# Kernel tuning notes

Hardware: AMD Instinct MI355X
Metric: run time of the kernel (lower is better)

Reference implementation:

```python
import jax, jax.numpy as jnp
import numpy as np

L = 5          # num_layer
D = 256        # emb_dim
N = 50000      # nodes
E = 800000     # edges
NUM_ATOM_FEATS, ATOM_VOCAB = 9, 120
NUM_BOND_FEATS, BOND_VOCAB = 3, 6
BN_EPS = 1e-5


def setup_inputs() -> dict:
    key = jax.random.key(0)
    ks = jax.random.split(key, 16)
    s = 0.02
    inp = {
        "x": jax.random.randint(ks[0], (N, NUM_ATOM_FEATS), 0, ATOM_VOCAB),
        "edge_index": jax.random.randint(ks[1], (2, E), 0, N),
        "edge_attr": jax.random.randint(ks[2], (E, NUM_BOND_FEATS), 0, BOND_VOCAB),
        "atom_emb": jax.random.normal(ks[3], (NUM_ATOM_FEATS, ATOM_VOCAB, D), jnp.float32) * s,
        "bond_emb": jax.random.normal(ks[4], (L, NUM_BOND_FEATS, BOND_VOCAB, D), jnp.float32) * s,
        "eps": jnp.zeros((L,), jnp.float32),
        "W1": jax.random.normal(ks[5], (L, D, 2 * D), jnp.float32) * s,
        "b1": jnp.zeros((L, 2 * D), jnp.float32),
        "g1": jnp.ones((L, 2 * D), jnp.float32),
        "be1": jnp.zeros((L, 2 * D), jnp.float32),
        "W2": jax.random.normal(ks[6], (L, 2 * D, D), jnp.float32) * s,
        "b2": jnp.zeros((L, D), jnp.float32),
        "g2": jnp.ones((L, D), jnp.float32),
        "be2": jnp.zeros((L, D), jnp.float32),
    }
    return inp


def _batchnorm(h, g, b):
    # training-mode BatchNorm1d over the node dimension
    m = jnp.mean(h, axis=0)
    v = jnp.mean(jnp.square(h - m), axis=0)
    return (h - m) * jax.lax.rsqrt(v + BN_EPS) * g + b


def reference(x, edge_index, edge_attr, atom_emb, bond_emb, eps,
              W1, b1, g1, be1, W2, b2, g2, be2):
    # AtomEncoder: sum of per-feature embedding lookups -> [N, D]
    h = jnp.sum(
        jnp.stack([atom_emb[f][x[:, f]] for f in range(NUM_ATOM_FEATS)], 0), 0)
    src, dst = edge_index[0], edge_index[1]
    for l in range(L):
        # BondEncoder for this layer -> [E, D]
        e = jnp.sum(jnp.stack(
            [bond_emb[l, f][edge_attr[:, f]] for f in range(NUM_BOND_FEATS)], 0), 0)
        msg = jax.nn.relu(h[src] + e)                          # gather + transform
        agg = jax.ops.segment_sum(msg, dst, num_segments=N)   # scatter-add
        z = (1.0 + eps[l]) * h + agg
        z = _batchnorm(z @ W1[l] + b1[l], g1[l], be1[l])       # MLP hidden + BN
        z = jax.nn.relu(z) @ W2[l] + b2[l]
        z = _batchnorm(z, g2[l], be2[l])                       # outer BN
        if l < L - 1:
            z = jax.nn.relu(z)
        h = z
    return h  # JK='last', drop_ratio=0
```

## Files before the change

### kernel.cpp

```cpp
#include <hip/hip_runtime.h>
#include <stdint.h>

#define NODES 50000
#define EDGES 800000
#define EMB   256
#define MPAD  50048
#define BNEPS 1e-5f
#define SCANB 196

typedef unsigned short u16;
typedef unsigned int   u32;
typedef _Float16 f16;
typedef __attribute__((ext_vector_type(4))) _Float16 f16x4;
typedef __attribute__((ext_vector_type(8))) _Float16 f16x8;
typedef __attribute__((ext_vector_type(4))) float f32x4;


__global__ void k_w1t(const float* __restrict__ W1, f16* __restrict__ Wt){
  int i = blockIdx.x * 256 + threadIdx.x;
  if (i >= 5*512*256) return;
  int k = i & 255, n = (i >> 8) & 511, l = i >> 17;
  Wt[i] = (f16)W1[((size_t)l << 17) + ((size_t)k << 9) + n];
}
__global__ void k_w2t(const float* __restrict__ W2, f16* __restrict__ Wt){
  int i = blockIdx.x * 256 + threadIdx.x;
  if (i >= 5*256*512) return;
  int k = i & 511, n = (i >> 9) & 255, l = i >> 17;
  Wt[i] = (f16)W2[((size_t)l << 17) + ((size_t)k << 8) + n];
}

__global__ void k_ebond(const float* __restrict__ bemb, f16* __restrict__ eb){
  int l = blockIdx.x / 216, p = blockIdx.x % 216;
  int a0 = p % 6, a1 = (p / 6) % 6, a2 = p / 36;
  int d0 = threadIdx.x * 4;
  const float* b = bemb + (size_t)l * 3 * 6 * 256;
  float4 v0 = *(const float4*)(b + (0*6 + a0)*256 + d0);
  float4 v1 = *(const float4*)(b + (1*6 + a1)*256 + d0);
  float4 v2 = *(const float4*)(b + (2*6 + a2)*256 + d0);
  f16x4 o = {(f16)(v0.x+v1.x+v2.x), (f16)(v0.y+v1.y+v2.y),
             (f16)(v0.z+v1.z+v2.z), (f16)(v0.w+v1.w+v2.w)};
  *(f16x4*)(eb + (((size_t)l*216 + p) << 8) + d0) = o;
}

__global__ void k_atom(const int* __restrict__ x, const float* __restrict__ aemb,
                       f16* __restrict__ h){
  int n = blockIdx.x * 4 + (threadIdx.x >> 6);
  int lane = threadIdx.x & 63;
  if (n >= NODES) return;
  int d0 = lane * 4;
  float a0=0.f, a1=0.f, a2=0.f, a3=0.f;
#pragma unroll
  for (int f = 0; f < 9; ++f){
    int v = x[n*9 + f];
    float4 e = *(const float4*)(aemb + (((size_t)f*120 + v) << 8) + d0);
    a0 += e.x; a1 += e.y; a2 += e.z; a3 += e.w;
  }
  f16x4 o = {(f16)a0, (f16)a1, (f16)a2, (f16)a3};
  *(f16x4*)(h + (size_t)n*EMB + d0) = o;
}


__global__ void k_hist(const int* __restrict__ dst, int* __restrict__ counts){
  int e = blockIdx.x * 256 + threadIdx.x;
  if (e < EDGES) atomicAdd(&counts[dst[e]], 1);
}

__global__ void k_bsum(const int* __restrict__ counts, int* __restrict__ bsums){
  __shared__ int red[256];
  int t = threadIdx.x;
  int i = blockIdx.x * 256 + t;
  red[t] = (i < NODES) ? counts[i] : 0;
  __syncthreads();
  for (int off = 128; off > 0; off >>= 1){
    if (t < off) red[t] += red[t + off];
    __syncthreads();
  }
  if (t == 0) bsums[blockIdx.x] = red[0];
}

__global__ void k_bscan(int* __restrict__ bsums){
  __shared__ int sc[256];
  int t = threadIdx.x;
  int v = (t < SCANB) ? bsums[t] : 0;
  sc[t] = v;
  __syncthreads();
  for (int off = 1; off < 256; off <<= 1){
    int u = (t >= off) ? sc[t - off] : 0;
    __syncthreads();
    sc[t] += u;
    __syncthreads();
  }
  if (t < SCANB) bsums[t] = sc[t] - v;
}

__global__ void k_fill(const int* __restrict__ counts, const int* __restrict__ bsums,
                       int* __restrict__ rs, int* __restrict__ fill){
  __shared__ int sc[256];
  int t = threadIdx.x;
  int i = blockIdx.x * 256 + t;
  int v = (i < NODES) ? counts[i] : 0;
  sc[t] = v;
  __syncthreads();
  for (int off = 1; off < 256; off <<= 1){
    int u = (t >= off) ? sc[t - off] : 0;
    __syncthreads();
    sc[t] += u;
    __syncthreads();
  }
  if (i < NODES){
    int e = bsums[blockIdx.x] + sc[t] - v;
    rs[i] = e; fill[i] = e;
    if (i == NODES - 1) rs[NODES] = e + v;
  }
}

__global__ void k_scatter(const int* __restrict__ src, const int* __restrict__ dst,
                          const int* __restrict__ ea, int* __restrict__ fill,
                          int* __restrict__ csrc, int* __restrict__ cattr){
  int e = blockIdx.x * 256 + threadIdx.x;
  if (e >= EDGES) return;
  int d = dst[e];
  int p = atomicAdd(&fill[d], 1);
  csrc[p]  = src[e];
  cattr[p] = ea[e*3+0] + 6*ea[e*3+1] + 36*ea[e*3+2];
}


__global__ void k_gather(const f16* __restrict__ h, const f16* __restrict__ ebl,
                         const int* __restrict__ rs, const int* __restrict__ csrc,
                         const int* __restrict__ cattr, const float* __restrict__ epsv,
                         int layer, f16* __restrict__ z){
  int n = blockIdx.x * 4 + (threadIdx.x >> 6);
  int lane = threadIdx.x & 63;
  int half = lane >> 5;
  int dl = (lane & 31) * 8;
  if (n >= MPAD) return;
  if (n >= NODES){
    if (half == 0){
      f16x8 zz = {(f16)0.f,(f16)0.f,(f16)0.f,(f16)0.f,(f16)0.f,(f16)0.f,(f16)0.f,(f16)0.f};
      *(f16x8*)(z + (size_t)n*EMB + dl) = zz;
    }
    return;
  }
  float acc[8];
#pragma unroll
  for (int k = 0; k < 8; ++k) acc[k] = 0.f;
  int i1 = rs[n+1];
  int i  = rs[n] + half;
  bool v = i < i1;
  int s = 0, pa = 0;
  if (v){ s = csrc[i]; pa = cattr[i]; }
  while (v){
    f16x8 hv = *(const f16x8*)(h + (size_t)s*EMB + dl);
    f16x8 ev = *(const f16x8*)(ebl + ((size_t)pa << 8) + dl);
    int in = i + 2;
    bool vn = in < i1;
    int sn = 0, pan = 0;
    if (vn){ sn = csrc[in]; pan = cattr[in]; }
#pragma unroll
    for (int k = 0; k < 8; ++k)
      acc[k] += fmaxf((float)hv[k] + (float)ev[k], 0.f);
    i = in; s = sn; pa = pan; v = vn;
  }
#pragma unroll
  for (int k = 0; k < 8; ++k) acc[k] += __shfl_xor(acc[k], 32);
  if (half == 0){
    float ep = 1.0f + epsv[layer];
    f16x8 hv = *(const f16x8*)(h + (size_t)n*EMB + dl);
    f16x8 o;
#pragma unroll
    for (int k = 0; k < 8; ++k) o[k] = (f16)(acc[k] + ep*(float)hv[k]);
    *(f16x8*)(z + (size_t)n*EMB + dl) = o;
  }
}

template<int K, int NCOL, bool FUSEBN>
__global__ __launch_bounds__(256)
void k_gemm(const f16* __restrict__ A, const f16* __restrict__ Bt,
            const f16* __restrict__ bnsc, const f16* __restrict__ bnsh,
            f16* __restrict__ C, float* __restrict__ csum, float* __restrict__ csq){
  const int tid  = threadIdx.x;
  const int lane = tid & 63;
  const int wid  = tid >> 6;
  const int bm0 = blockIdx.x * 128;
  const int bn0 = blockIdx.y * 128;
  const int wm = (wid >> 1) * 64;
  const int wn = (wid & 1) * 64;
  const int lr = lane & 15;
  const int kc = (lane >> 4) * 8;

  const f16* Ap = A  + (size_t)(bm0 + wm + lr)*K + kc;
  const f16* Bp = Bt + (size_t)(bn0 + wn + lr)*K + kc;

  f32x4 acc[4][4];
#pragma unroll
  for (int m = 0; m < 4; ++m)
#pragma unroll
    for (int n = 0; n < 4; ++n) acc[m][n] = (f32x4){0.f,0.f,0.f,0.f};

  const f16x8 zero8 = {(f16)0.f,(f16)0.f,(f16)0.f,(f16)0.f,
                       (f16)0.f,(f16)0.f,(f16)0.f,(f16)0.f};

#pragma unroll 2
  for (int kk = 0; kk < K/32; ++kk){
    f16x8 af[4], bf[4];
#pragma unroll
    for (int m = 0; m < 4; ++m)
      af[m] = *(const f16x8*)(Ap + (size_t)m*16*K + kk*32);
#pragma unroll
    for (int n = 0; n < 4; ++n)
      bf[n] = *(const f16x8*)(Bp + (size_t)n*16*K + kk*32);
    if (FUSEBN){
      f16x8 sc = *(const f16x8*)(bnsc + kk*32 + kc);
      f16x8 sh = *(const f16x8*)(bnsh + kk*32 + kc);
#pragma unroll
      for (int m = 0; m < 4; ++m){
        f16x8 t = af[m]*sc + sh;
#pragma unroll
        for (int j = 0; j < 8; ++j) t[j] = (t[j] > (f16)0.f) ? t[j] : (f16)0.f;
        af[m] = (bm0 + wm + m*16 + lr < NODES) ? t : zero8;
      }
    }
#pragma unroll
    for (int m = 0; m < 4; ++m)
#pragma unroll
      for (int n = 0; n < 4; ++n)
        acc[m][n] = __builtin_amdgcn_mfma_f32_16x16x32_f16(af[m], bf[n], acc[m][n], 0, 0, 0);
  }

  const int r0 = (lane >> 4) * 4;
  const int cc = lane & 15;
#pragma unroll
  for (int m = 0; m < 4; ++m)
#pragma unroll
    for (int n = 0; n < 4; ++n)
#pragma unroll
      for (int j = 0; j < 4; ++j){
        int row = bm0 + wm + m*16 + r0 + j;
        int col = bn0 + wn + n*16 + cc;
        C[(size_t)row*NCOL + col] = (f16)acc[m][n][j];
      }
#pragma unroll
  for (int n = 0; n < 4; ++n){
    float s = 0.f, q = 0.f;
#pragma unroll
    for (int m = 0; m < 4; ++m)
#pragma unroll
      for (int j = 0; j < 4; ++j){ float v = acc[m][n][j]; s += v; q += v*v; }
    s += __shfl_xor(s, 16); q += __shfl_xor(q, 16);
    s += __shfl_xor(s, 32); q += __shfl_xor(q, 32);
    if (lane < 16){
      atomicAdd(csum + bn0 + wn + n*16 + cc, s);
      atomicAdd(csq  + bn0 + wn + n*16 + cc, q);
    }
  }
}

__global__ void k_finalize(const float* __restrict__ sum, const float* __restrict__ sumsq,
                           const float* __restrict__ g, const float* __restrict__ be,
                           float* __restrict__ scale, float* __restrict__ shift,
                           f16* __restrict__ scf, f16* __restrict__ shf, int nc){
  int c = blockIdx.x * 256 + threadIdx.x;
  if (c >= nc) return;
  float m = sum[c] * (1.0f / NODES);
  float v = sumsq[c] * (1.0f / NODES) - m*m;
  float sc = rsqrtf(v + BNEPS) * g[c];
  float sh = be[c] - m*sc;
  scale[c] = sc;  shift[c] = sh;
  scf[c] = (f16)sc;  shf[c] = (f16)sh;
}

__global__ void k_apply2(const f16* __restrict__ zp, const float* __restrict__ scale,
                         const float* __restrict__ shift, f16* __restrict__ hout,
                         float* __restrict__ fout, int dorelu){
  int idx = blockIdx.x * 256 + threadIdx.x;
  int row = idx >> 5;
  int c0  = (idx & 31) * 8;
  if (row >= NODES) return;
  size_t off = (size_t)row * EMB + c0;
  f16x8 v = *(const f16x8*)(zp + off);
  float4 sA = *(const float4*)(scale + c0), sB = *(const float4*)(scale + c0 + 4);
  float4 tA = *(const float4*)(shift + c0), tB = *(const float4*)(shift + c0 + 4);
  float r0 = (float)v[0]*sA.x + tA.x;
  float r1 = (float)v[1]*sA.y + tA.y;
  float r2 = (float)v[2]*sA.z + tA.z;
  float r3 = (float)v[3]*sA.w + tA.w;
  float r4 = (float)v[4]*sB.x + tB.x;
  float r5 = (float)v[5]*sB.y + tB.y;
  float r6 = (float)v[6]*sB.z + tB.z;
  float r7 = (float)v[7]*sB.w + tB.w;
  if (dorelu){
    r0=fmaxf(r0,0.f); r1=fmaxf(r1,0.f); r2=fmaxf(r2,0.f); r3=fmaxf(r3,0.f);
    r4=fmaxf(r4,0.f); r5=fmaxf(r5,0.f); r6=fmaxf(r6,0.f); r7=fmaxf(r7,0.f);
  }
  if (fout){
    float4 f0 = {r0,r1,r2,r3}, f1 = {r4,r5,r6,r7};
    float* q = fout + off;
    *(float4*)q = f0; *(float4*)(q + 4) = f1;
  } else {
    f16x8 o = {(f16)r0,(f16)r1,(f16)r2,(f16)r3,(f16)r4,(f16)r5,(f16)r6,(f16)r7};
    *(f16x8*)(hout + off) = o;
  }
}


extern "C" void kernel_launch(void* const* d_in, const int* in_sizes, int n_in,
                              void* d_out, int out_size, void* d_ws, size_t ws_size,
                              hipStream_t stream){
  const int*   x    = (const int*)  d_in[0];
  const int*   ei   = (const int*)  d_in[1];
  const int*   ea   = (const int*)  d_in[2];
  const float* aemb = (const float*)d_in[3];
  const float* bemb = (const float*)d_in[4];
  const float* epsv = (const float*)d_in[5];
  const float* W1   = (const float*)d_in[6];
  const float* g1   = (const float*)d_in[8];
  const float* be1  = (const float*)d_in[9];
  const float* W2   = (const float*)d_in[10];
  const float* g2   = (const float*)d_in[12];
  const float* be2  = (const float*)d_in[13];
  float* out = (float*)d_out;

  char* p = (char*)d_ws;
  auto take = [&](size_t bytes){ char* r = p; p += (bytes + 255) & ~(size_t)255; return r; };
  f16* h      = (f16*)take((size_t)NODES*EMB*2);
  f16* z      = (f16*)take((size_t)MPAD*EMB*2);
  f16* hidden = (f16*)take((size_t)MPAD*512*2);
  f16* W1t    = (f16*)take((size_t)5*512*256*2);
  f16* W2t    = (f16*)take((size_t)5*256*512*2);
  f16* eb     = (f16*)take((size_t)5*216*256*2);
  float* stats= (float*)take((size_t)4*512*4);
  float* csum = stats, *csq = stats + 512, *scale = stats + 1024, *shift = stats + 1536;
  f16* scf    = (f16*)take((size_t)512*2);
  f16* shf    = (f16*)take((size_t)512*2);
  int* counts = (int*)take((size_t)NODES*4);
  int* rs     = (int*)take((size_t)(NODES+1)*4);
  int* fill   = (int*)take((size_t)NODES*4);
  int* bsums  = (int*)take((size_t)SCANB*4);
  int* csrc   = (int*)take((size_t)EDGES*4);
  int* cattr  = (int*)take((size_t)EDGES*4);

  k_w1t<<<2560, 256, 0, stream>>>(W1, W1t);
  k_w2t<<<2560, 256, 0, stream>>>(W2, W2t);
  k_ebond<<<5*216, 64, 0, stream>>>(bemb, eb);
  k_atom<<<12500, 256, 0, stream>>>(x, aemb, h);
  hipMemsetAsync(counts, 0, (size_t)NODES*4, stream);
  k_hist<<<EDGES/256, 256, 0, stream>>>(ei + EDGES, counts);
  k_bsum<<<SCANB, 256, 0, stream>>>(counts, bsums);
  k_bscan<<<1, 256, 0, stream>>>(bsums);
  k_fill<<<SCANB, 256, 0, stream>>>(counts, bsums, rs, fill);
  k_scatter<<<EDGES/256, 256, 0, stream>>>(ei, ei + EDGES, ea, fill, csrc, cattr);

  for (int l = 0; l < 5; ++l){
    k_gather<<<MPAD/4, 256, 0, stream>>>(h, eb + (size_t)l*216*256, rs, csrc, cattr, epsv, l, z);
    hipMemsetAsync(stats, 0, 2*512*4, stream);
    k_gemm<256,512,false><<<dim3(MPAD/128, 4), 256, 0, stream>>>(
        z, W1t + (size_t)l*512*256, nullptr, nullptr, hidden, csum, csq);
    k_finalize<<<2, 256, 0, stream>>>(csum, csq, g1 + l*512, be1 + l*512,
                                      scale, shift, scf, shf, 512);
    hipMemsetAsync(stats, 0, 2*512*4, stream);
    k_gemm<512,256,true><<<dim3(MPAD/128, 2), 256, 0, stream>>>(
        hidden, W2t + (size_t)l*256*512, scf, shf, z, csum, csq);
    k_finalize<<<1, 256, 0, stream>>>(csum, csq, g2 + l*256, be2 + l*256,
                                      scale, shift, scf, shf, 256);
    if (l < 4)
      k_apply2<<<NODES*32/256, 256, 0, stream>>>(z, scale, shift, h, nullptr, 1);
    else
      k_apply2<<<NODES*32/256, 256, 0, stream>>>(z, scale, shift, nullptr, out, 0);
  }
}
```

Baseline: 1.424 ms.

## Stage GEMM tiles in LDS via direct global-to-LDS loads with XOR swizzle

The GEMM kernel used to load its A and B fragments straight from global memory into registers for each wave, so waves sharing a tile fetched the same rows more than once. It now loads 128x64 tiles of A and B into shared memory with global_load_lds, using an XOR swizzle on 16-byte chunks to avoid bank conflicts. MFMA fragments are then read from LDS. The goal is better data reuse and coalesced loads, at the cost of two barriers per k-tile and no double buffering, so load latency is not overlapped with compute.

New measurement: 1.188 ms. -16.6%, faster.

```diff
diff --git a/kernel.cpp b/kernel.cpp
--- a/kernel.cpp
+++ b/kernel.cpp
@@ -14,6 +14,11 @@
 typedef __attribute__((ext_vector_type(4))) _Float16 f16x4;
 typedef __attribute__((ext_vector_type(8))) _Float16 f16x8;
 typedef __attribute__((ext_vector_type(4))) float f32x4;
+
+__device__ __forceinline__ void gload16(const void* g, void* l){
+  __builtin_amdgcn_global_load_lds((const __attribute__((address_space(1))) void*)g,
+                                   (__attribute__((address_space(3))) void*)l, 16, 0, 0);
+}
 
 
 __global__ void k_w1t(const float* __restrict__ W1, f16* __restrict__ Wt){
@@ -179,6 +184,8 @@
 void k_gemm(const f16* __restrict__ A, const f16* __restrict__ Bt,
             const f16* __restrict__ bnsc, const f16* __restrict__ bnsh,
             f16* __restrict__ C, float* __restrict__ csum, float* __restrict__ csq){
+  __shared__ __align__(16) u16 As[128*64];
+  __shared__ __align__(16) u16 Bs[128*64];
   const int tid  = threadIdx.x;
   const int lane = tid & 63;
   const int wid  = tid >> 6;
@@ -186,11 +193,6 @@
   const int bn0 = blockIdx.y * 128;
   const int wm = (wid >> 1) * 64;
   const int wn = (wid & 1) * 64;
-  const int lr = lane & 15;
-  const int kc = (lane >> 4) * 8;
-
-  const f16* Ap = A  + (size_t)(bm0 + wm + lr)*K + kc;
-  const f16* Bp = Bt + (size_t)(bn0 + wn + lr)*K + kc;
 
   f32x4 acc[4][4];
 #pragma unroll
@@ -201,31 +203,51 @@
   const f16x8 zero8 = {(f16)0.f,(f16)0.f,(f16)0.f,(f16)0.f,
                        (f16)0.f,(f16)0.f,(f16)0.f,(f16)0.f};
 
-#pragma unroll 2
-  for (int kk = 0; kk < K/32; ++kk){
-    f16x8 af[4], bf[4];
-#pragma unroll
-    for (int m = 0; m < 4; ++m)
-      af[m] = *(const f16x8*)(Ap + (size_t)m*16*K + kk*32);
-#pragma unroll
-    for (int n = 0; n < 4; ++n)
-      bf[n] = *(const f16x8*)(Bp + (size_t)n*16*K + kk*32);
-    if (FUSEBN){
-      f16x8 sc = *(const f16x8*)(bnsc + kk*32 + kc);
-      f16x8 sh = *(const f16x8*)(bnsh + kk*32 + kc);
+  for (int kt = 0; kt < K/64; ++kt){
+    __syncthreads();
+#pragma unroll
+    for (int it = 0; it < 4; ++it){
+      int tix = tid + it*256;
+      int r = tix >> 3;
+      int c = tix & 7;
+      int sc = c ^ (r & 7);
+      gload16(A  + (size_t)(bm0 + r)*K + kt*64 + sc*8, (char*)As + tix*16);
+      gload16(Bt + (size_t)(bn0 + r)*K + kt*64 + sc*8, (char*)Bs + tix*16);
+    }
+    __syncthreads();
+#pragma unroll
+    for (int kk = 0; kk < 2; ++kk){
+      f16x8 af[4], bfr[4];
 #pragma unroll
       for (int m = 0; m < 4; ++m){
-        f16x8 t = af[m]*sc + sh;
-#pragma unroll
-        for (int j = 0; j < 8; ++j) t[j] = (t[j] > (f16)0.f) ? t[j] : (f16)0.f;
-        af[m] = (bm0 + wm + m*16 + lr < NODES) ? t : zero8;
+        int row = wm + m*16 + (lane & 15);
+        int phys = (kk*4 + (lane >> 4)) ^ (row & 7);
+        af[m] = *(const f16x8*)((const char*)As + row*128 + phys*16);
       }
+#pragma unroll
+      for (int n = 0; n < 4; ++n){
+        int row = wn + n*16 + (lane & 15);
+        int phys = (kk*4 + (lane >> 4)) ^ (row & 7);
+        bfr[n] = *(const f16x8*)((const char*)Bs + row*128 + phys*16);
+      }
+      if (FUSEBN){
+        int kb = kt*64 + (kk*4 + (lane >> 4))*8;
+        f16x8 sc = *(const f16x8*)(bnsc + kb);
+        f16x8 sh = *(const f16x8*)(bnsh + kb);
+#pragma unroll
+        for (int m = 0; m < 4; ++m){
+          f16x8 t = af[m]*sc + sh;
+#pragma unroll
+          for (int j = 0; j < 8; ++j) t[j] = (t[j] > (f16)0.f) ? t[j] : (f16)0.f;
+          af[m] = (bm0 + wm + m*16 + (lane & 15) < NODES) ? t : zero8;
+        }
+      }
+#pragma unroll
+      for (int m = 0; m < 4; ++m)
+#pragma unroll
+        for (int n = 0; n < 4; ++n)
+          acc[m][n] = __builtin_amdgcn_mfma_f32_16x16x32_f16(af[m], bfr[n], acc[m][n], 0, 0, 0);
     }
-#pragma unroll
-    for (int m = 0; m < 4; ++m)
-#pragma unroll
-      for (int n = 0; n < 4; ++n)
-        acc[m][n] = __builtin_amdgcn_mfma_f32_16x16x32_f16(af[m], bf[n], acc[m][n], 0, 0, 0);
   }
 
   const int r0 = (lane >> 4) * 4;
```
